# Kernel tuning notes

Hardware: AMD Instinct MI355X
Metric: run time of the kernel (lower is better)

## Reference

```python
import jax, jax.numpy as jnp
import numpy as np

B, S, D, H = 4, 2048, 1024, 16
DH = D // H


def setup_inputs() -> dict:
    key = jax.random.key(0)
    kq, kk, kv, kw, kb = jax.random.split(key, 5)
    queries = jax.random.normal(kq, (B, S, D), dtype=jnp.float32)
    keys = jax.random.normal(kk, (B, S, D), dtype=jnp.float32)
    values = jax.random.normal(kv, (B, S, D), dtype=jnp.float32)
    # True = masked-out padding position; mask the last 64 keys of batch 0
    kpm = np.zeros((B, S), dtype=bool)
    kpm[0, -64:] = True
    key_padding_mask = jnp.asarray(kpm)
    W_O = jax.random.normal(kw, (D, D), dtype=jnp.float32) / np.sqrt(D)
    b_O = jax.random.normal(kb, (D,), dtype=jnp.float32) * 0.01
    return {"queries": queries, "keys": keys, "values": values,
            "key_padding_mask": key_padding_mask, "W_O": W_O, "b_O": b_O}


def reference(queries, keys, values, key_padding_mask, W_O, b_O):
    batch, len_q, d_model = queries.shape
    len_k = keys.shape[1]
    # [B, H, S, DH]
    q = queries.reshape(batch, len_q, H, DH).transpose(0, 2, 1, 3)
    k = keys.reshape(batch, len_k, H, DH).transpose(0, 2, 1, 3)
    v = values.reshape(batch, len_k, H, DH).transpose(0, 2, 1, 3)
    sim = jnp.einsum('bhqd,bhkd->bhqk', q, k) / jnp.sqrt(jnp.float32(DH))
    neg_inf = jnp.finfo(sim.dtype).min
    # padding mask: True means masked
    sim = jnp.where(key_padding_mask[:, None, None, :], neg_inf, sim)
    # causal mask (is_causal=True)
    causal = jnp.tril(jnp.ones((len_q, len_k), dtype=bool))
    sim = jnp.where(causal[None, None], sim, neg_inf)
    attn = jax.nn.softmax(sim, axis=-1)
    out = jnp.einsum('bhqk,bhkd->bhqd', attn, v)  # [B, H, Sq, DH]
    out = out.transpose(0, 2, 1, 3).reshape(batch, len_q, d_model)
    return out @ W_O.T + b_O
```

## Files before the change

kernel.cpp:

```cpp
#include <hip/hip_runtime.h>
#include <hip/hip_bf16.h>

#define B_ 4
#define S_ 2048
#define D_ 1024
#define H_ 16
#define DH_ 64

typedef __attribute__((ext_vector_type(8))) short bf16x8;
typedef __attribute__((ext_vector_type(4))) float f32x4;
typedef __attribute__((ext_vector_type(16))) float f32x16;
typedef __attribute__((ext_vector_type(2))) int v2i;
typedef unsigned int uint32;

__device__ __forceinline__ unsigned short f2bf(float f) {
  unsigned int u = __float_as_uint(f);
  u += 0x7FFFu + ((u >> 16) & 1u);
  return (unsigned short)(u >> 16);
}

__device__ __forceinline__ uint32 pk2(float lo, float hi) {
  return __builtin_amdgcn_perm(__float_as_uint(hi), __float_as_uint(lo), 0x07060302u);
}

__device__ __forceinline__ float half_add(float v) {
  v2i r = __builtin_amdgcn_permlane32_swap(__float_as_int(v), __float_as_int(v), false, false);
  return __int_as_float(r[0]) + __int_as_float(r[1]);
}

__global__ void prep_kernel(const float* __restrict__ k, const float* __restrict__ w,
                            const int* __restrict__ kpm, const float* __restrict__ v,
                            ushort* __restrict__ Kb, ushort* __restrict__ Wb,
                            float* __restrict__ MF, int* __restrict__ anyM,
                            ushort* __restrict__ Vt) {
  __shared__ ushort tile[64][68];
  const int bid = blockIdx.x;
  const int t = threadIdx.x;
  if (bid < 8192) {
    int i = bid * 256 + t;
    float4 a = ((const float4*)k)[i];
    ushort4 r;
    r.x = f2bf(a.x); r.y = f2bf(a.y); r.z = f2bf(a.z); r.w = f2bf(a.w);
    ((ushort4*)Kb)[i] = r;
  } else if (bid < 9216) {
    int i = (bid - 8192) * 256 + t;
    float4 a = ((const float4*)w)[i];
    ushort4 r;
    r.x = f2bf(a.x); r.y = f2bf(a.y); r.z = f2bf(a.z); r.w = f2bf(a.w);
    ((ushort4*)Wb)[i] = r;
  } else if (bid < 9248) {
    int i = (bid - 9216) * 256 + t;
    int m = kpm[i];
    MF[i] = m ? -1e30f : 0.0f;
    unsigned long long bal = __ballot(m != 0);
    if ((i & 63) == 0) anyM[i >> 6] = (bal != 0ull) ? 1 : 0;
  } else {
    int bx = bid - 9248;
    int bh = bx >> 5;
    int s0 = (bx & 31) << 6;
    int b = bh >> 4, h = bh & 15;
#pragma unroll
    for (int it = 0; it < 16; ++it) {
      int r = it * 4 + (t >> 6);
      int c = t & 63;
      float x = v[(size_t)(b * S_ + s0 + r) * D_ + h * DH_ + c];
      tile[r][c] = f2bf(x);
    }
    __syncthreads();
#pragma unroll
    for (int it = 0; it < 16; ++it) {
      int d = it * 4 + (t >> 6);
      int s = t & 63;
      Vt[(size_t)(bh * DH_ + d) * S_ + s0 + s] = tile[s][d];
    }
  }
}

__global__ __launch_bounds__(256, 2) void attn_fwd(
    const float* __restrict__ q, const ushort* __restrict__ Kb,
    const ushort* __restrict__ Vt, const float* __restrict__ MF,
    const int* __restrict__ anyM, ushort* __restrict__ AO) {
  __shared__ ushort Klds[2][2][64 * 64];
  __shared__ ushort Vlds[2][2][64 * 64];

  const int d_ = blockIdx.x;
  const int l_ = (d_ & 7) * 64 + (d_ >> 3);
  const int xx = l_ & 7;
  const int h = (l_ >> 3) & 15;
  const int b = l_ >> 7;

  const int tid = threadIdx.x;
  const int wv = tid >> 6, ln = tid & 63;
  const int q32 = ln & 31;
  const int hi = ln >> 5;
  const int l7 = ln & 7, l3 = ln >> 3;
  const float SC = 0.18033688011112042f;
  const int cr4 = 4 * hi;

  const ushort* Kg = Kb + (size_t)b * S_ * D_ + h * DH_;
  const ushort* Vg = Vt + (size_t)((b * H_ + h) * DH_) * S_;

  bf16x8 kst[4], vst[4];
  const int wrow0 = 16 * wv + l3;
  const int wss = (l7 ^ l3) * 8;

  f32x16 zz;
#pragma unroll
  for (int i = 0; i < 16; ++i) zz[i] = 0.f;

  auto loadTile = [&](int kt) {
#pragma unroll
    for (int hh = 0; hh < 2; ++hh)
#pragma unroll
      for (int p = 0; p < 2; ++p) {
        int row = wrow0 + 8 * p;
        kst[2 * hh + p] = *(const bf16x8*)(Kg + (size_t)(kt * 128 + hh * 64 + row) * D_ + l7 * 8);
        vst[2 * hh + p] = *(const bf16x8*)(Vg + (size_t)row * S_ + kt * 128 + hh * 64 + l7 * 8);
      }
  };
  auto writeTile = [&](int buf) {
#pragma unroll
    for (int hh = 0; hh < 2; ++hh)
#pragma unroll
      for (int p = 0; p < 2; ++p) {
        int row = wrow0 + 8 * p;
        *(bf16x8*)(&Klds[buf][hh][row * 64 + wss]) = kst[2 * hh + p];
        *(bf16x8*)(&Vlds[buf][hh][row * 64 + wss]) = vst[2 * hh + p];
      }
  };
  auto packTile = [&](const f32x16& pv, bf16x8* out) {
#pragma unroll
    for (int kk = 0; kk < 2; ++kk) {
      uint32 a  = pk2(pv[8 * kk + 0], pv[8 * kk + 1]);
      uint32 c  = pk2(pv[8 * kk + 2], pv[8 * kk + 3]);
      uint32 bb = pk2(pv[8 * kk + 4], pv[8 * kk + 5]);
      uint32 dd = pk2(pv[8 * kk + 6], pv[8 * kk + 7]);
      v2i r0 = __builtin_amdgcn_permlane32_swap((int)a, (int)bb, false, false);
      v2i r1 = __builtin_amdgcn_permlane32_swap((int)c, (int)dd, false, false);
      union { uint32 u[4]; bf16x8 v; } w;
      w.u[0] = (uint32)r0[0]; w.u[1] = (uint32)r1[0];
      w.u[2] = (uint32)r0[1]; w.u[3] = (uint32)r1[1];
      out[kk] = w.v;
    }
  };

  for (int half = 0; half < 2; ++half) {
    const int q0 = (half ? (15 - xx) : xx) * 128;
    const int qw0 = q0 + wv * 32;
    const int qb = qw0 >> 5;

    bf16x8 qf[4];
    {
      const float* qp = q + (size_t)(b * S_ + qw0 + q32) * D_ + h * DH_ + hi * 8;
#pragma unroll
      for (int j = 0; j < 4; ++j) {
        float4 x0 = *(const float4*)(qp + 16 * j);
        float4 x1 = *(const float4*)(qp + 16 * j + 4);
        bf16x8 t;
        t[0] = (short)f2bf(x0.x * SC); t[1] = (short)f2bf(x0.y * SC);
        t[2] = (short)f2bf(x0.z * SC); t[3] = (short)f2bf(x0.w * SC);
        t[4] = (short)f2bf(x1.x * SC); t[5] = (short)f2bf(x1.y * SC);
        t[6] = (short)f2bf(x1.z * SC); t[7] = (short)f2bf(x1.w * SC);
        qf[j] = t;
      }
    }

    f32x16 ot0, ot1;
#pragma unroll
    for (int i = 0; i < 16; ++i) { ot0[i] = 0.f; ot1[i] = 0.f; }
    float l_run = 0.f;

    auto full64 = [&](int cur, int hh) {
      const ushort* Kl = &Klds[cur][hh][0];
      const ushort* Vl = &Vlds[cur][hh][0];
      f32x16 s0v, s1v;
      __builtin_amdgcn_s_setprio(1);
#pragma unroll
      for (int j = 0; j < 4; ++j) {
        bf16x8 kf = *(const bf16x8*)(&Kl[q32 * 64 + (((2 * j + hi) ^ l7) * 8)]);
        s0v = __builtin_amdgcn_mfma_f32_32x32x16_bf16(kf, qf[j], j ? s0v : zz, 0, 0, 0);
      }
#pragma unroll
      for (int j = 0; j < 4; ++j) {
        bf16x8 kf = *(const bf16x8*)(&Kl[(32 + q32) * 64 + (((2 * j + hi) ^ l7) * 8)]);
        s1v = __builtin_amdgcn_mfma_f32_32x32x16_bf16(kf, qf[j], j ? s1v : zz, 0, 0, 0);
      }
      __builtin_amdgcn_s_setprio(0);
      float rsa = 0.f, rsb = 0.f;
#pragma unroll
      for (int r = 0; r < 16; ++r) {
        float p0 = __builtin_amdgcn_exp2f(s0v[r]); s0v[r] = p0;
        float p1 = __builtin_amdgcn_exp2f(s1v[r]); s1v[r] = p1;
        if (r & 1) { rsb += p0; rsb += p1; } else { rsa += p0; rsa += p1; }
      }
      l_run += half_add(rsa + rsb);

      bf16x8 pa[4];
      packTile(s0v, &pa[0]);
      packTile(s1v, &pa[2]);
      __builtin_amdgcn_s_setprio(1);
#pragma unroll
      for (int dt = 0; dt < 2; ++dt) {
        f32x16& ot = dt ? ot1 : ot0;
        const int rowb = (dt * 32 + q32) * 64;
        bf16x8 v0 = *(const bf16x8*)(&Vl[rowb + (((0 + hi) ^ l7) * 8)]);
        ot = __builtin_amdgcn_mfma_f32_32x32x16_bf16(v0, pa[0], ot, 0, 0, 0);
        bf16x8 v1 = *(const bf16x8*)(&Vl[rowb + (((2 + hi) ^ l7) * 8)]);
        ot = __builtin_amdgcn_mfma_f32_32x32x16_bf16(v1, pa[1], ot, 0, 0, 0);
        bf16x8 v2 = *(const bf16x8*)(&Vl[rowb + (((4 + hi) ^ l7) * 8)]);
        ot = __builtin_amdgcn_mfma_f32_32x32x16_bf16(v2, pa[2], ot, 0, 0, 0);
        bf16x8 v3 = *(const bf16x8*)(&Vl[rowb + (((6 + hi) ^ l7) * 8)]);
        ot = __builtin_amdgcn_mfma_f32_32x32x16_bf16(v3, pa[3], ot, 0, 0, 0);
      }
      __builtin_amdgcn_s_setprio(0);
    };

    auto generic64 = [&](int t64, int cur, int hh) {
      const int k0 = t64 * 64;
      const ushort* Kl = &Klds[cur][hh][0];
      const ushort* Vl = &Vlds[cur][hh][0];
      const bool a0 = (2 * t64) <= qb, a1 = (2 * t64 + 1) <= qb;
      if (!(a0 || a1)) return;
      const bool dg0 = (2 * t64) == qb, dg1 = (2 * t64 + 1) == qb;
      const int flag = anyM[b * 32 + t64];

      f32x16 s0v, s1v;
      __builtin_amdgcn_s_setprio(1);
      if (a0) {
#pragma unroll
        for (int j = 0; j < 4; ++j) {
          bf16x8 kf = *(const bf16x8*)(&Kl[q32 * 64 + (((2 * j + hi) ^ l7) * 8)]);
          s0v = __builtin_amdgcn_mfma_f32_32x32x16_bf16(kf, qf[j], j ? s0v : zz, 0, 0, 0);
        }
      }
      if (a1) {
#pragma unroll
        for (int j = 0; j < 4; ++j) {
          bf16x8 kf = *(const bf16x8*)(&Kl[(32 + q32) * 64 + (((2 * j + hi) ^ l7) * 8)]);
          s1v = __builtin_amdgcn_mfma_f32_32x32x16_bf16(kf, qf[j], j ? s1v : zz, 0, 0, 0);
        }
      }
      __builtin_amdgcn_s_setprio(0);

      float rsa = 0.f, rsb = 0.f;
      if (a0) {
#pragma unroll
        for (int r = 0; r < 16; ++r) {
          int cr = (r & 3) + 8 * (r >> 2) + cr4;
          float s = s0v[r];
          if (flag) s += MF[b * S_ + k0 + cr];
          if (dg0 && cr > q32) s = -3.0e38f;
          float p = __builtin_amdgcn_exp2f(s);
          s0v[r] = p;
          if (r & 1) rsb += p; else rsa += p;
        }
      }
      if (a1) {
#pragma unroll
        for (int r = 0; r < 16; ++r) {
          int cr = (r & 3) + 8 * (r >> 2) + cr4;
          float s = s1v[r];
          if (flag) s += MF[b * S_ + k0 + 32 + cr];
          if (dg1 && cr > q32) s = -3.0e38f;
          float p = __builtin_amdgcn_exp2f(s);
          s1v[r] = p;
          if (r & 1) rsb += p; else rsa += p;
        }
      }
      l_run += half_add(rsa + rsb);

      bf16x8 pa[4];
      if (a0) packTile(s0v, &pa[0]);
      if (a1) packTile(s1v, &pa[2]);

      __builtin_amdgcn_s_setprio(1);
#pragma unroll
      for (int dt = 0; dt < 2; ++dt) {
        f32x16& ot = dt ? ot1 : ot0;
        const int rowb = (dt * 32 + q32) * 64;
        if (a0) {
          bf16x8 v0 = *(const bf16x8*)(&Vl[rowb + (((0 + hi) ^ l7) * 8)]);
          ot = __builtin_amdgcn_mfma_f32_32x32x16_bf16(v0, pa[0], ot, 0, 0, 0);
          bf16x8 v1 = *(const bf16x8*)(&Vl[rowb + (((2 + hi) ^ l7) * 8)]);
          ot = __builtin_amdgcn_mfma_f32_32x32x16_bf16(v1, pa[1], ot, 0, 0, 0);
        }
        if (a1) {
          bf16x8 v2 = *(const bf16x8*)(&Vl[rowb + (((4 + hi) ^ l7) * 8)]);
          ot = __builtin_amdgcn_mfma_f32_32x32x16_bf16(v2, pa[2], ot, 0, 0, 0);
          bf16x8 v3 = *(const bf16x8*)(&Vl[rowb + (((6 + hi) ^ l7) * 8)]);
          ot = __builtin_amdgcn_mfma_f32_32x32x16_bf16(v3, pa[3], ot, 0, 0, 0);
        }
      }
      __builtin_amdgcn_s_setprio(0);
    };

    const int M = (q0 >> 7) + 1;
    loadTile(0);
    writeTile(0);
    if (M > 1) loadTile(1);
    __syncthreads();

    for (int tt = 0; tt < M; ++tt) {
      const int cur = tt & 1;
      if (tt + 1 < M) writeTile(cur ^ 1);
      if (tt + 2 < M) loadTile(tt + 2);
      if (tt < M - 1) {
        const int f0 = anyM[b * 32 + 2 * tt] | anyM[b * 32 + 2 * tt + 1];
        if (f0) { generic64(2 * tt, cur, 0); generic64(2 * tt + 1, cur, 1); }
        else { full64(cur, 0); full64(cur, 1); }
      } else {
        generic64(2 * tt, cur, 0);
        generic64(2 * tt + 1, cur, 1);
      }
      __syncthreads();
    }

    const float inv = __builtin_amdgcn_rcpf(l_run);
    ushort* tb = ((ushort*)Klds) + wv * 2048;
#pragma unroll
    for (int dt = 0; dt < 2; ++dt) {
      const f32x16& ot = dt ? ot1 : ot0;
#pragma unroll
      for (int rp = 0; rp < 8; ++rp) {
        int r0 = rp * 2;
        int d0 = dt * 32 + (r0 & 3) + 8 * (r0 >> 2) + cr4;
        uint32 w = pk2(ot[r0] * inv, ot[r0 + 1] * inv);
        int e = q32 * 64 + (((d0 >> 3) ^ (q32 & 7)) * 8) + (d0 & 7);
        *(uint32*)(&tb[e]) = w;
      }
    }
    __syncthreads();
#pragma unroll
    for (int it = 0; it < 4; ++it) {
      int qq = it * 8 + l3;
      bf16x8 val = *(const bf16x8*)(&tb[qq * 64 + ((l7 ^ (qq & 7)) * 8)]);
      *(bf16x8*)(AO + (size_t)(b * S_ + qw0 + qq) * D_ + h * DH_ + l7 * 8) = val;
    }
    __syncthreads();
  }
}

__global__ __launch_bounds__(256, 2) void gemm_out(
    const ushort* __restrict__ A, const ushort* __restrict__ Wb,
    const float* __restrict__ bO, float* __restrict__ out) {
  __shared__ ushort Al[2][128 * 64];
  __shared__ ushort Wl[2][128 * 64];
  const int dd = blockIdx.x;
  const int m0 = (dd & 63) * 128;
  const int n0 = (dd >> 6) * 128;
  const int tid = threadIdx.x;
  const int wv = tid >> 6, ln = tid & 63;
  const int r16 = ln & 15, g = ln >> 4;
  const int wm = wv >> 1, wn = wv & 1;
  const int trow = tid >> 3, tslot = tid & 7;
  f32x4 acc[4][4] = {};
  bf16x8 ast[4], wst[4];

  auto stageReg = [&](int kc) {
    const int kk = kc * 64;
#pragma unroll
    for (int p = 0; p < 4; ++p) {
      int row = trow + 32 * p;
      ast[p] = *(const bf16x8*)(A + (size_t)(m0 + row) * D_ + kk + tslot * 8);
      wst[p] = *(const bf16x8*)(Wb + (size_t)(n0 + row) * D_ + kk + tslot * 8);
    }
  };
  auto writeL = [&](int buf) {
#pragma unroll
    for (int p = 0; p < 4; ++p) {
      int row = trow + 32 * p;
      int soff = (tslot ^ (row & 7)) * 8;
      *(bf16x8*)(&Al[buf][row * 64 + soff]) = ast[p];
      *(bf16x8*)(&Wl[buf][row * 64 + soff]) = wst[p];
    }
  };

  stageReg(0);
  writeL(0);
  stageReg(1);
  __syncthreads();

  for (int kc = 0; kc < 16; ++kc) {
    const int cur = kc & 1;
    if (kc + 1 < 16) writeL(cur ^ 1);
    if (kc + 2 < 16) stageReg(kc + 2);
#pragma unroll
    for (int hh = 0; hh < 2; ++hh) {
      bf16x8 af[4], wf[4];
#pragma unroll
      for (int m = 0; m < 4; ++m) {
        int row = 64 * wm + 16 * m + r16;
        af[m] = *(const bf16x8*)(&Al[cur][row * 64 + (((4 * hh + g) ^ (row & 7)) * 8)]);
      }
#pragma unroll
      for (int n = 0; n < 4; ++n) {
        int row = 64 * wn + 16 * n + r16;
        wf[n] = *(const bf16x8*)(&Wl[cur][row * 64 + (((4 * hh + g) ^ (row & 7)) * 8)]);
      }
#pragma unroll
      for (int m = 0; m < 4; ++m)
#pragma unroll
        for (int n = 0; n < 4; ++n)
          acc[m][n] = __builtin_amdgcn_mfma_f32_16x16x32_bf16(af[m], wf[n], acc[m][n], 0, 0, 0);
    }
    __syncthreads();
  }

#pragma unroll
  for (int n = 0; n < 4; ++n) {
    float bb = bO[n0 + 32 * wn * 2 + 16 * n + r16];
#pragma unroll
    for (int m = 0; m < 4; ++m) {
#pragma unroll
      for (int j = 0; j < 4; ++j) {
        out[(size_t)(m0 + 64 * wm + 16 * m + 4 * g + j) * D_ + n0 + 64 * wn + 16 * n + r16] =
            acc[m][n][j] + bb;
      }
    }
  }
}

extern "C" void kernel_launch(void* const* d_in, const int* in_sizes, int n_in,
                              void* d_out, int out_size, void* d_ws, size_t ws_size,
                              hipStream_t stream) {
  const float* q = (const float*)d_in[0];
  const float* k = (const float*)d_in[1];
  const float* v = (const float*)d_in[2];
  const int* kpm = (const int*)d_in[3];
  const float* W = (const float*)d_in[4];
  const float* bO = (const float*)d_in[5];

  char* ws = (char*)d_ws;
  const size_t SZ = (size_t)B_ * S_ * D_ * 2;
  ushort* Kb = (ushort*)ws;
  ushort* Vt = (ushort*)(ws + SZ);
  ushort* AO = (ushort*)(ws + 2 * SZ);
  ushort* Wb = (ushort*)(ws + 3 * SZ);
  float* MF = (float*)(ws + 3 * SZ + (size_t)D_ * D_ * 2);
  int* anyM = (int*)(ws + 3 * SZ + (size_t)D_ * D_ * 2 + (size_t)B_ * S_ * 4);

  prep_kernel<<<11296, 256, 0, stream>>>(k, W, kpm, v, Kb, Wb, MF, anyM, Vt);
  attn_fwd<<<512, 256, 0, stream>>>(q, Kb, Vt, MF, anyM, AO);
  gemm_out<<<512, 256, 0, stream>>>(AO, Wb, bO, (float*)d_out);
}
```

Baseline: 96.17 us.

## Split paired causal query tiles into separate blocks with 64-key tiles

Each attention block previously handled two query tiles, an early one paired with a late one for causal load balance, and streamed 128-key tiles. Now each of 1024 blocks handles one query tile, ordered from longest to shortest, and streams 64-key double-buffered tiles, which halves shared memory per block. This is meant to raise occupancy and parallelism and to let the scheduler balance the uneven causal work, at the cost of more blocks and more barriers per key step. The gemm bias index expression is also rewritten to an equivalent form.

```diff
diff --git a/kernel.cpp b/kernel.cpp
--- a/kernel.cpp
+++ b/kernel.cpp
@@ -80,14 +80,15 @@
     const float* __restrict__ q, const ushort* __restrict__ Kb,
     const ushort* __restrict__ Vt, const float* __restrict__ MF,
     const int* __restrict__ anyM, ushort* __restrict__ AO) {
-  __shared__ ushort Klds[2][2][64 * 64];
-  __shared__ ushort Vlds[2][2][64 * 64];
+  __shared__ ushort Klds[2][64 * 64];
+  __shared__ ushort Vlds[2][64 * 64];
 
   const int d_ = blockIdx.x;
-  const int l_ = (d_ & 7) * 64 + (d_ >> 3);
-  const int xx = l_ & 7;
-  const int h = (l_ >> 3) & 15;
-  const int b = l_ >> 7;
+  const int l_ = (d_ & 7) * 128 + (d_ >> 3);
+  const int xx = l_ & 15;
+  const int h = (l_ >> 4) & 15;
+  const int b = l_ >> 8;
+  const int q0 = (15 - xx) * 128;
 
   const int tid = threadIdx.x;
   const int wv = tid >> 6, ln = tid & 63;
@@ -100,7 +101,7 @@
   const ushort* Kg = Kb + (size_t)b * S_ * D_ + h * DH_;
   const ushort* Vg = Vt + (size_t)((b * H_ + h) * DH_) * S_;
 
-  bf16x8 kst[4], vst[4];
+  bf16x8 kst[2], vst[2];
   const int wrow0 = 16 * wv + l3;
   const int wss = (l7 ^ l3) * 8;
 
@@ -110,23 +111,19 @@
 
   auto loadTile = [&](int kt) {
 #pragma unroll
-    for (int hh = 0; hh < 2; ++hh)
-#pragma unroll
-      for (int p = 0; p < 2; ++p) {
-        int row = wrow0 + 8 * p;
-        kst[2 * hh + p] = *(const bf16x8*)(Kg + (size_t)(kt * 128 + hh * 64 + row) * D_ + l7 * 8);
-        vst[2 * hh + p] = *(const bf16x8*)(Vg + (size_t)row * S_ + kt * 128 + hh * 64 + l7 * 8);
-      }
+    for (int p = 0; p < 2; ++p) {
+      int row = wrow0 + 8 * p;
+      kst[p] = *(const bf16x8*)(Kg + (size_t)(kt * 64 + row) * D_ + l7 * 8);
+      vst[p] = *(const bf16x8*)(Vg + (size_t)row * S_ + kt * 64 + l7 * 8);
+    }
   };
   auto writeTile = [&](int buf) {
 #pragma unroll
-    for (int hh = 0; hh < 2; ++hh)
-#pragma unroll
-      for (int p = 0; p < 2; ++p) {
-        int row = wrow0 + 8 * p;
-        *(bf16x8*)(&Klds[buf][hh][row * 64 + wss]) = kst[2 * hh + p];
-        *(bf16x8*)(&Vlds[buf][hh][row * 64 + wss]) = vst[2 * hh + p];
-      }
+    for (int p = 0; p < 2; ++p) {
+      int row = wrow0 + 8 * p;
+      *(bf16x8*)(&Klds[buf][row * 64 + wss]) = kst[p];
+      *(bf16x8*)(&Vlds[buf][row * 64 + wss]) = vst[p];
+    }
   };
   auto packTile = [&](const f32x16& pv, bf16x8* out) {
 #pragma unroll
@@ -144,199 +141,193 @@
     }
   };
 
-  for (int half = 0; half < 2; ++half) {
-    const int q0 = (half ? (15 - xx) : xx) * 128;
-    const int qw0 = q0 + wv * 32;
-    const int qb = qw0 >> 5;
-
-    bf16x8 qf[4];
-    {
-      const float* qp = q + (size_t)(b * S_ + qw0 + q32) * D_ + h * DH_ + hi * 8;
-#pragma unroll
-      for (int j = 0; j < 4; ++j) {
-        float4 x0 = *(const float4*)(qp + 16 * j);
-        float4 x1 = *(const float4*)(qp + 16 * j + 4);
-        bf16x8 t;
-        t[0] = (short)f2bf(x0.x * SC); t[1] = (short)f2bf(x0.y * SC);
-        t[2] = (short)f2bf(x0.z * SC); t[3] = (short)f2bf(x0.w * SC);
-        t[4] = (short)f2bf(x1.x * SC); t[5] = (short)f2bf(x1.y * SC);
-        t[6] = (short)f2bf(x1.z * SC); t[7] = (short)f2bf(x1.w * SC);
-        qf[j] = t;
-      }
-    }
-
-    f32x16 ot0, ot1;
-#pragma unroll
-    for (int i = 0; i < 16; ++i) { ot0[i] = 0.f; ot1[i] = 0.f; }
-    float l_run = 0.f;
-
-    auto full64 = [&](int cur, int hh) {
-      const ushort* Kl = &Klds[cur][hh][0];
-      const ushort* Vl = &Vlds[cur][hh][0];
-      f32x16 s0v, s1v;
-      __builtin_amdgcn_s_setprio(1);
+  const int qw0 = q0 + wv * 32;
+  const int qb = qw0 >> 5;
+
+  bf16x8 qf[4];
+  {
+    const float* qp = q + (size_t)(b * S_ + qw0 + q32) * D_ + h * DH_ + hi * 8;
+#pragma unroll
+    for (int j = 0; j < 4; ++j) {
+      float4 x0 = *(const float4*)(qp + 16 * j);
+      float4 x1 = *(const float4*)(qp + 16 * j + 4);
+      bf16x8 t;
+      t[0] = (short)f2bf(x0.x * SC); t[1] = (short)f2bf(x0.y * SC);
+      t[2] = (short)f2bf(x0.z * SC); t[3] = (short)f2bf(x0.w * SC);
+      t[4] = (short)f2bf(x1.x * SC); t[5] = (short)f2bf(x1.y * SC);
+      t[6] = (short)f2bf(x1.z * SC); t[7] = (short)f2bf(x1.w * SC);
+      qf[j] = t;
+    }
+  }
+
+  f32x16 ot0, ot1;
+#pragma unroll
+  for (int i = 0; i < 16; ++i) { ot0[i] = 0.f; ot1[i] = 0.f; }
+  float l_run = 0.f;
+
+  auto full64 = [&](int cur) {
+    const ushort* Kl = &Klds[cur][0];
+    const ushort* Vl = &Vlds[cur][0];
+    f32x16 s0v, s1v;
+    __builtin_amdgcn_s_setprio(1);
+#pragma unroll
+    for (int j = 0; j < 4; ++j) {
+      bf16x8 kf = *(const bf16x8*)(&Kl[q32 * 64 + (((2 * j + hi) ^ l7) * 8)]);
+      s0v = __builtin_amdgcn_mfma_f32_32x32x16_bf16(kf, qf[j], j ? s0v : zz, 0, 0, 0);
+    }
+#pragma unroll
+    for (int j = 0; j < 4; ++j) {
+      bf16x8 kf = *(const bf16x8*)(&Kl[(32 + q32) * 64 + (((2 * j + hi) ^ l7) * 8)]);
+      s1v = __builtin_amdgcn_mfma_f32_32x32x16_bf16(kf, qf[j], j ? s1v : zz, 0, 0, 0);
+    }
+    __builtin_amdgcn_s_setprio(0);
+    float rsa = 0.f, rsb = 0.f;
+#pragma unroll
+    for (int r = 0; r < 16; ++r) {
+      float p0 = __builtin_amdgcn_exp2f(s0v[r]); s0v[r] = p0;
+      float p1 = __builtin_amdgcn_exp2f(s1v[r]); s1v[r] = p1;
+      if (r & 1) { rsb += p0; rsb += p1; } else { rsa += p0; rsa += p1; }
+    }
+    l_run += half_add(rsa + rsb);
+
+    bf16x8 pa[4];
+    packTile(s0v, &pa[0]);
+    packTile(s1v, &pa[2]);
+    __builtin_amdgcn_s_setprio(1);
+#pragma unroll
+    for (int dt = 0; dt < 2; ++dt) {
+      f32x16& ot = dt ? ot1 : ot0;
+      const int rowb = (dt * 32 + q32) * 64;
+      bf16x8 v0 = *(const bf16x8*)(&Vl[rowb + (((0 + hi) ^ l7) * 8)]);
+      ot = __builtin_amdgcn_mfma_f32_32x32x16_bf16(v0, pa[0], ot, 0, 0, 0);
+      bf16x8 v1 = *(const bf16x8*)(&Vl[rowb + (((2 + hi) ^ l7) * 8)]);
+      ot = __builtin_amdgcn_mfma_f32_32x32x16_bf16(v1, pa[1], ot, 0, 0, 0);
+      bf16x8 v2 = *(const bf16x8*)(&Vl[rowb + (((4 + hi) ^ l7) * 8)]);
+      ot = __builtin_amdgcn_mfma_f32_32x32x16_bf16(v2, pa[2], ot, 0, 0, 0);
+      bf16x8 v3 = *(const bf16x8*)(&Vl[rowb + (((6 + hi) ^ l7) * 8)]);
+      ot = __builtin_amdgcn_mfma_f32_32x32x16_bf16(v3, pa[3], ot, 0, 0, 0);
+    }
+    __builtin_amdgcn_s_setprio(0);
+  };
+
+  auto generic64 = [&](int t64, int cur) {
+    const int k0 = t64 * 64;
+    const ushort* Kl = &Klds[cur][0];
+    const ushort* Vl = &Vlds[cur][0];
+    const bool a0 = (2 * t64) <= qb, a1 = (2 * t64 + 1) <= qb;
+    if (!(a0 || a1)) return;
+    const bool dg0 = (2 * t64) == qb, dg1 = (2 * t64 + 1) == qb;
+    const int flag = anyM[b * 32 + t64];
+
+    f32x16 s0v, s1v;
+    __builtin_amdgcn_s_setprio(1);
+    if (a0) {
 #pragma unroll
       for (int j = 0; j < 4; ++j) {
         bf16x8 kf = *(const bf16x8*)(&Kl[q32 * 64 + (((2 * j + hi) ^ l7) * 8)]);
         s0v = __builtin_amdgcn_mfma_f32_32x32x16_bf16(kf, qf[j], j ? s0v : zz, 0, 0, 0);
       }
+    }
+    if (a1) {
 #pragma unroll
       for (int j = 0; j < 4; ++j) {
         bf16x8 kf = *(const bf16x8*)(&Kl[(32 + q32) * 64 + (((2 * j + hi) ^ l7) * 8)]);
         s1v = __builtin_amdgcn_mfma_f32_32x32x16_bf16(kf, qf[j], j ? s1v : zz, 0, 0, 0);
       }
-      __builtin_amdgcn_s_setprio(0);
-      float rsa = 0.f, rsb = 0.f;
+    }
+    __builtin_amdgcn_s_setprio(0);
+
+    float rsa = 0.f, rsb = 0.f;
+    if (a0) {
 #pragma unroll
       for (int r = 0; r < 16; ++r) {
-        float p0 = __builtin_amdgcn_exp2f(s0v[r]); s0v[r] = p0;
-        float p1 = __builtin_amdgcn_exp2f(s1v[r]); s1v[r] = p1;
-        if (r & 1) { rsb += p0; rsb += p1; } else { rsa += p0; rsa += p1; }
-      }
-      l_run += half_add(rsa + rsb);
-
-      bf16x8 pa[4];
-      packTile(s0v, &pa[0]);
-      packTile(s1v, &pa[2]);
-      __builtin_amdgcn_s_setprio(1);
-#pragma unroll
-      for (int dt = 0; dt < 2; ++dt) {
-        f32x16& ot = dt ? ot1 : ot0;
-        const int rowb = (dt * 32 + q32) * 64;
+        int cr = (r & 3) + 8 * (r >> 2) + cr4;
+        float s = s0v[r];
+        if (flag) s += MF[b * S_ + k0 + cr];
+        if (dg0 && cr > q32) s = -3.0e38f;
+        float p = __builtin_amdgcn_exp2f(s);
+        s0v[r] = p;
+        if (r & 1) rsb += p; else rsa += p;
+      }
+    }
+    if (a1) {
+#pragma unroll
+      for (int r = 0; r < 16; ++r) {
+        int cr = (r & 3) + 8 * (r >> 2) + cr4;
+        float s = s1v[r];
+        if (flag) s += MF[b * S_ + k0 + 32 + cr];
+        if (dg1 && cr > q32) s = -3.0e38f;
+        float p = __builtin_amdgcn_exp2f(s);
+        s1v[r] = p;
+        if (r & 1) rsb += p; else rsa += p;
+      }
+    }
+    l_run += half_add(rsa + rsb);
+
+    bf16x8 pa[4];
+    if (a0) packTile(s0v, &pa[0]);
+    if (a1) packTile(s1v, &pa[2]);
+
+    __builtin_amdgcn_s_setprio(1);
+#pragma unroll
+    for (int dt = 0; dt < 2; ++dt) {
+      f32x16& ot = dt ? ot1 : ot0;
+      const int rowb = (dt * 32 + q32) * 64;
+      if (a0) {
         bf16x8 v0 = *(const bf16x8*)(&Vl[rowb + (((0 + hi) ^ l7) * 8)]);
         ot = __builtin_amdgcn_mfma_f32_32x32x16_bf16(v0, pa[0], ot, 0, 0, 0);
         bf16x8 v1 = *(const bf16x8*)(&Vl[rowb + (((2 + hi) ^ l7) * 8)]);
         ot = __builtin_amdgcn_mfma_f32_32x32x16_bf16(v1, pa[1], ot, 0, 0, 0);
+      }
+      if (a1) {
         bf16x8 v2 = *(const bf16x8*)(&Vl[rowb + (((4 + hi) ^ l7) * 8)]);
         ot = __builtin_amdgcn_mfma_f32_32x32x16_bf16(v2, pa[2], ot, 0, 0, 0);
         bf16x8 v3 = *(const bf16x8*)(&Vl[rowb + (((6 + hi) ^ l7) * 8)]);
         ot = __builtin_amdgcn_mfma_f32_32x32x16_bf16(v3, pa[3], ot, 0, 0, 0);
       }
-      __builtin_amdgcn_s_setprio(0);
-    };
-
-    auto generic64 = [&](int t64, int cur, int hh) {
-      const int k0 = t64 * 64;
-      const ushort* Kl = &Klds[cur][hh][0];
-      const ushort* Vl = &Vlds[cur][hh][0];
-      const bool a0 = (2 * t64) <= qb, a1 = (2 * t64 + 1) <= qb;
-      if (!(a0 || a1)) return;
-      const bool dg0 = (2 * t64) == qb, dg1 = (2 * t64 + 1) == qb;
-      const int flag = anyM[b * 32 + t64];
-
-      f32x16 s0v, s1v;
-      __builtin_amdgcn_s_setprio(1);
-      if (a0) {
-#pragma unroll
-        for (int j = 0; j < 4; ++j) {
-          bf16x8 kf = *(const bf16x8*)(&Kl[q32 * 64 + (((2 * j + hi) ^ l7) * 8)]);
-          s0v = __builtin_amdgcn_mfma_f32_32x32x16_bf16(kf, qf[j], j ? s0v : zz, 0, 0, 0);
-        }
-      }
-      if (a1) {
-#pragma unroll
-        for (int j = 0; j < 4; ++j) {
-          bf16x8 kf = *(const bf16x8*)(&Kl[(32 + q32) * 64 + (((2 * j + hi) ^ l7) * 8)]);
-          s1v = __builtin_amdgcn_mfma_f32_32x32x16_bf16(kf, qf[j], j ? s1v : zz, 0, 0, 0);
-        }
-      }
-      __builtin_amdgcn_s_setprio(0);
-
-      float rsa = 0.f, rsb = 0.f;
-      if (a0) {
-#pragma unroll
-        for (int r = 0; r < 16; ++r) {
-          int cr = (r & 3) + 8 * (r >> 2) + cr4;
-          float s = s0v[r];
-          if (flag) s += MF[b * S_ + k0 + cr];
-          if (dg0 && cr > q32) s = -3.0e38f;
-          float p = __builtin_amdgcn_exp2f(s);
-          s0v[r] = p;
-          if (r & 1) rsb += p; else rsa += p;
-        }
-      }
-      if (a1) {
-#pragma unroll
-        for (int r = 0; r < 16; ++r) {
-          int cr = (r & 3) + 8 * (r >> 2) + cr4;
-          float s = s1v[r];
-          if (flag) s += MF[b * S_ + k0 + 32 + cr];
-          if (dg1 && cr > q32) s = -3.0e38f;
-          float p = __builtin_amdgcn_exp2f(s);
-          s1v[r] = p;
-          if (r & 1) rsb += p; else rsa += p;
-        }
-      }
-      l_run += half_add(rsa + rsb);
-
-      bf16x8 pa[4];
-      if (a0) packTile(s0v, &pa[0]);
-      if (a1) packTile(s1v, &pa[2]);
-
-      __builtin_amdgcn_s_setprio(1);
-#pragma unroll
-      for (int dt = 0; dt < 2; ++dt) {
-        f32x16& ot = dt ? ot1 : ot0;
-        const int rowb = (dt * 32 + q32) * 64;
-        if (a0) {
-          bf16x8 v0 = *(const bf16x8*)(&Vl[rowb + (((0 + hi) ^ l7) * 8)]);
-          ot = __builtin_amdgcn_mfma_f32_32x32x16_bf16(v0, pa[0], ot, 0, 0, 0);
-          bf16x8 v1 = *(const bf16x8*)(&Vl[rowb + (((2 + hi) ^ l7) * 8)]);
-          ot = __builtin_amdgcn_mfma_f32_32x32x16_bf16(v1, pa[1], ot, 0, 0, 0);
-        }
-        if (a1) {
-          bf16x8 v2 = *(const bf16x8*)(&Vl[rowb + (((4 + hi) ^ l7) * 8)]);
-          ot = __builtin_amdgcn_mfma_f32_32x32x16_bf16(v2, pa[2], ot, 0, 0, 0);
-          bf16x8 v3 = *(const bf16x8*)(&Vl[rowb + (((6 + hi) ^ l7) * 8)]);
-          ot = __builtin_amdgcn_mfma_f32_32x32x16_bf16(v3, pa[3], ot, 0, 0, 0);
-        }
-      }
-      __builtin_amdgcn_s_setprio(0);
-    };
-
-    const int M = (q0 >> 7) + 1;
-    loadTile(0);
-    writeTile(0);
-    if (M > 1) loadTile(1);
+    }
+    __builtin_amdgcn_s_setprio(0);
+  };
+
+  const int nkb = (q0 >> 6) + 2;
+  loadTile(0);
+  writeTile(0);
+  loadTile(1);
+  __syncthreads();
+
+  for (int t = 0; t < nkb; ++t) {
+    const int cur = t & 1;
+    if (t + 1 < nkb) writeTile(cur ^ 1);
+    if (t + 2 < nkb) loadTile(t + 2);
+    if (t < nkb - 2) {
+      if (anyM[b * 32 + t]) generic64(t, cur);
+      else full64(cur);
+    } else {
+      generic64(t, cur);
+    }
     __syncthreads();
-
-    for (int tt = 0; tt < M; ++tt) {
-      const int cur = tt & 1;
-      if (tt + 1 < M) writeTile(cur ^ 1);
-      if (tt + 2 < M) loadTile(tt + 2);
-      if (tt < M - 1) {
-        const int f0 = anyM[b * 32 + 2 * tt] | anyM[b * 32 + 2 * tt + 1];
-        if (f0) { generic64(2 * tt, cur, 0); generic64(2 * tt + 1, cur, 1); }
-        else { full64(cur, 0); full64(cur, 1); }
-      } else {
-        generic64(2 * tt, cur, 0);
-        generic64(2 * tt + 1, cur, 1);
-      }
-      __syncthreads();
-    }
-
-    const float inv = __builtin_amdgcn_rcpf(l_run);
-    ushort* tb = ((ushort*)Klds) + wv * 2048;
-#pragma unroll
-    for (int dt = 0; dt < 2; ++dt) {
-      const f32x16& ot = dt ? ot1 : ot0;
-#pragma unroll
-      for (int rp = 0; rp < 8; ++rp) {
-        int r0 = rp * 2;
-        int d0 = dt * 32 + (r0 & 3) + 8 * (r0 >> 2) + cr4;
-        uint32 w = pk2(ot[r0] * inv, ot[r0 + 1] * inv);
-        int e = q32 * 64 + (((d0 >> 3) ^ (q32 & 7)) * 8) + (d0 & 7);
-        *(uint32*)(&tb[e]) = w;
-      }
-    }
-    __syncthreads();
-#pragma unroll
-    for (int it = 0; it < 4; ++it) {
-      int qq = it * 8 + l3;
-      bf16x8 val = *(const bf16x8*)(&tb[qq * 64 + ((l7 ^ (qq & 7)) * 8)]);
-      *(bf16x8*)(AO + (size_t)(b * S_ + qw0 + qq) * D_ + h * DH_ + l7 * 8) = val;
-    }
-    __syncthreads();
+  }
+
+  const float inv = __builtin_amdgcn_rcpf(l_run);
+  ushort* tb = ((ushort*)Klds) + wv * 2048;
+#pragma unroll
+  for (int dt = 0; dt < 2; ++dt) {
+    const f32x16& ot = dt ? ot1 : ot0;
+#pragma unroll
+    for (int rp = 0; rp < 8; ++rp) {
+      int r0 = rp * 2;
+      int d0 = dt * 32 + (r0 & 3) + 8 * (r0 >> 2) + cr4;
+      uint32 w = pk2(ot[r0] * inv, ot[r0 + 1] * inv);
+      int e = q32 * 64 + (((d0 >> 3) ^ (q32 & 7)) * 8) + (d0 & 7);
+      *(uint32*)(&tb[e]) = w;
+    }
+  }
+  __syncthreads();
+#pragma unroll
+  for (int it = 0; it < 4; ++it) {
+    int qq = it * 8 + l3;
+    bf16x8 val = *(const bf16x8*)(&tb[qq * 64 + ((l7 ^ (qq & 7)) * 8)]);
+    *(bf16x8*)(AO + (size_t)(b * S_ + qw0 + qq) * D_ + h * DH_ + l7 * 8) = val;
   }
 }
 
@@ -408,7 +399,7 @@
 
 #pragma unroll
   for (int n = 0; n < 4; ++n) {
-    float bb = bO[n0 + 32 * wn * 2 + 16 * n + r16];
+    float bb = bO[n0 + 64 * wn + 16 * n + r16];
 #pragma unroll
     for (int m = 0; m < 4; ++m) {
 #pragma unroll
@@ -440,6 +431,6 @@
   int* anyM = (int*)(ws + 3 * SZ + (size_t)D_ * D_ * 2 + (size_t)B_ * S_ * 4);
 
   prep_kernel<<<11296, 256, 0, stream>>>(k, W, kpm, v, Kb, Wb, MF, anyM, Vt);
-  attn_fwd<<<512, 256, 0, stream>>>(q, Kb, Vt, MF, anyM, AO);
+  attn_fwd<<<1024, 256, 0, stream>>>(q, Kb, Vt, MF, anyM, AO);
   gemm_out<<<512, 256, 0, stream>>>(AO, Wb, bO, (float*)d_out);
 }
```

After: 116.3 us. 21.0% more time.

## Process both paired causal query tiles in one K/V sweep

Applied to the files above, without the earlier changes.

The attention block previously handled its two query tiles (a short and a long causal row pair) in two sequential passes, loading K/V tiles twice. Now both Q tiles are kept in registers and a single pass over the longer tile's K/V range serves both, sharing each LDS tile load. This roughly halves K/V global loads and the barrier count per block, at the cost of doubling the output accumulator registers, which may reduce occupancy or cause spills. The bias index expression in the output GEMM is rewritten into an equivalent form.

```diff
diff --git a/kernel.cpp b/kernel.cpp
--- a/kernel.cpp
+++ b/kernel.cpp
@@ -144,182 +144,196 @@
     }
   };
 
-  for (int half = 0; half < 2; ++half) {
-    const int q0 = (half ? (15 - xx) : xx) * 128;
-    const int qw0 = q0 + wv * 32;
-    const int qb = qw0 >> 5;
-
-    bf16x8 qf[4];
-    {
-      const float* qp = q + (size_t)(b * S_ + qw0 + q32) * D_ + h * DH_ + hi * 8;
-#pragma unroll
-      for (int j = 0; j < 4; ++j) {
-        float4 x0 = *(const float4*)(qp + 16 * j);
-        float4 x1 = *(const float4*)(qp + 16 * j + 4);
-        bf16x8 t;
-        t[0] = (short)f2bf(x0.x * SC); t[1] = (short)f2bf(x0.y * SC);
-        t[2] = (short)f2bf(x0.z * SC); t[3] = (short)f2bf(x0.w * SC);
-        t[4] = (short)f2bf(x1.x * SC); t[5] = (short)f2bf(x1.y * SC);
-        t[6] = (short)f2bf(x1.z * SC); t[7] = (short)f2bf(x1.w * SC);
-        qf[j] = t;
-      }
-    }
-
-    f32x16 ot0, ot1;
-#pragma unroll
-    for (int i = 0; i < 16; ++i) { ot0[i] = 0.f; ot1[i] = 0.f; }
-    float l_run = 0.f;
-
-    auto full64 = [&](int cur, int hh) {
-      const ushort* Kl = &Klds[cur][hh][0];
-      const ushort* Vl = &Vlds[cur][hh][0];
-      f32x16 s0v, s1v;
-      __builtin_amdgcn_s_setprio(1);
+  const int q0A = xx * 128, q0B = (15 - xx) * 128;
+  const int qw0A = q0A + wv * 32, qw0B = q0B + wv * 32;
+  const int qbA = qw0A >> 5, qbB = qw0B >> 5;
+
+  bf16x8 qfA[4], qfB[4];
+  auto loadQ = [&](int qw0, bf16x8* qf) {
+    const float* qp = q + (size_t)(b * S_ + qw0 + q32) * D_ + h * DH_ + hi * 8;
+#pragma unroll
+    for (int j = 0; j < 4; ++j) {
+      float4 x0 = *(const float4*)(qp + 16 * j);
+      float4 x1 = *(const float4*)(qp + 16 * j + 4);
+      bf16x8 t;
+      t[0] = (short)f2bf(x0.x * SC); t[1] = (short)f2bf(x0.y * SC);
+      t[2] = (short)f2bf(x0.z * SC); t[3] = (short)f2bf(x0.w * SC);
+      t[4] = (short)f2bf(x1.x * SC); t[5] = (short)f2bf(x1.y * SC);
+      t[6] = (short)f2bf(x1.z * SC); t[7] = (short)f2bf(x1.w * SC);
+      qf[j] = t;
+    }
+  };
+  loadQ(qw0A, qfA);
+  loadQ(qw0B, qfB);
+
+  f32x16 oA0, oA1, oB0, oB1;
+#pragma unroll
+  for (int i = 0; i < 16; ++i) { oA0[i] = 0.f; oA1[i] = 0.f; oB0[i] = 0.f; oB1[i] = 0.f; }
+  float lA = 0.f, lB = 0.f;
+
+  auto fullG = [&](int cur, int hh, const bf16x8* qf, f32x16& o0, f32x16& o1, float& lr) {
+    const ushort* Kl = &Klds[cur][hh][0];
+    const ushort* Vl = &Vlds[cur][hh][0];
+    f32x16 s0v, s1v;
+    __builtin_amdgcn_s_setprio(1);
+#pragma unroll
+    for (int j = 0; j < 4; ++j) {
+      bf16x8 kf = *(const bf16x8*)(&Kl[q32 * 64 + (((2 * j + hi) ^ l7) * 8)]);
+      s0v = __builtin_amdgcn_mfma_f32_32x32x16_bf16(kf, qf[j], j ? s0v : zz, 0, 0, 0);
+    }
+#pragma unroll
+    for (int j = 0; j < 4; ++j) {
+      bf16x8 kf = *(const bf16x8*)(&Kl[(32 + q32) * 64 + (((2 * j + hi) ^ l7) * 8)]);
+      s1v = __builtin_amdgcn_mfma_f32_32x32x16_bf16(kf, qf[j], j ? s1v : zz, 0, 0, 0);
+    }
+    __builtin_amdgcn_s_setprio(0);
+    float rsa = 0.f, rsb = 0.f;
+#pragma unroll
+    for (int r = 0; r < 16; ++r) {
+      float p0 = __builtin_amdgcn_exp2f(s0v[r]); s0v[r] = p0;
+      float p1 = __builtin_amdgcn_exp2f(s1v[r]); s1v[r] = p1;
+      if (r & 1) { rsb += p0; rsb += p1; } else { rsa += p0; rsa += p1; }
+    }
+    lr += half_add(rsa + rsb);
+
+    bf16x8 pa[4];
+    packTile(s0v, &pa[0]);
+    packTile(s1v, &pa[2]);
+    __builtin_amdgcn_s_setprio(1);
+#pragma unroll
+    for (int dt = 0; dt < 2; ++dt) {
+      f32x16& ot = dt ? o1 : o0;
+      const int rowb = (dt * 32 + q32) * 64;
+      bf16x8 v0 = *(const bf16x8*)(&Vl[rowb + (((0 + hi) ^ l7) * 8)]);
+      ot = __builtin_amdgcn_mfma_f32_32x32x16_bf16(v0, pa[0], ot, 0, 0, 0);
+      bf16x8 v1 = *(const bf16x8*)(&Vl[rowb + (((2 + hi) ^ l7) * 8)]);
+      ot = __builtin_amdgcn_mfma_f32_32x32x16_bf16(v1, pa[1], ot, 0, 0, 0);
+      bf16x8 v2 = *(const bf16x8*)(&Vl[rowb + (((4 + hi) ^ l7) * 8)]);
+      ot = __builtin_amdgcn_mfma_f32_32x32x16_bf16(v2, pa[2], ot, 0, 0, 0);
+      bf16x8 v3 = *(const bf16x8*)(&Vl[rowb + (((6 + hi) ^ l7) * 8)]);
+      ot = __builtin_amdgcn_mfma_f32_32x32x16_bf16(v3, pa[3], ot, 0, 0, 0);
+    }
+    __builtin_amdgcn_s_setprio(0);
+  };
+
+  auto genericG = [&](int t64, int cur, int hh, const bf16x8* qf,
+                      f32x16& o0, f32x16& o1, float& lr, int qb) {
+    const int k0 = t64 * 64;
+    const ushort* Kl = &Klds[cur][hh][0];
+    const ushort* Vl = &Vlds[cur][hh][0];
+    const bool a0 = (2 * t64) <= qb, a1 = (2 * t64 + 1) <= qb;
+    if (!(a0 || a1)) return;
+    const bool dg0 = (2 * t64) == qb, dg1 = (2 * t64 + 1) == qb;
+    const int flag = anyM[b * 32 + t64];
+
+    f32x16 s0v, s1v;
+    __builtin_amdgcn_s_setprio(1);
+    if (a0) {
 #pragma unroll
       for (int j = 0; j < 4; ++j) {
         bf16x8 kf = *(const bf16x8*)(&Kl[q32 * 64 + (((2 * j + hi) ^ l7) * 8)]);
         s0v = __builtin_amdgcn_mfma_f32_32x32x16_bf16(kf, qf[j], j ? s0v : zz, 0, 0, 0);
       }
+    }
+    if (a1) {
 #pragma unroll
       for (int j = 0; j < 4; ++j) {
         bf16x8 kf = *(const bf16x8*)(&Kl[(32 + q32) * 64 + (((2 * j + hi) ^ l7) * 8)]);
         s1v = __builtin_amdgcn_mfma_f32_32x32x16_bf16(kf, qf[j], j ? s1v : zz, 0, 0, 0);
       }
-      __builtin_amdgcn_s_setprio(0);
-      float rsa = 0.f, rsb = 0.f;
+    }
+    __builtin_amdgcn_s_setprio(0);
+
+    float rsa = 0.f, rsb = 0.f;
+    if (a0) {
 #pragma unroll
       for (int r = 0; r < 16; ++r) {
-        float p0 = __builtin_amdgcn_exp2f(s0v[r]); s0v[r] = p0;
-        float p1 = __builtin_amdgcn_exp2f(s1v[r]); s1v[r] = p1;
-        if (r & 1) { rsb += p0; rsb += p1; } else { rsa += p0; rsa += p1; }
-      }
-      l_run += half_add(rsa + rsb);
-
-      bf16x8 pa[4];
-      packTile(s0v, &pa[0]);
-      packTile(s1v, &pa[2]);
-      __builtin_amdgcn_s_setprio(1);
-#pragma unroll
-      for (int dt = 0; dt < 2; ++dt) {
-        f32x16& ot = dt ? ot1 : ot0;
-        const int rowb = (dt * 32 + q32) * 64;
+        int cr = (r & 3) + 8 * (r >> 2) + cr4;
+        float s = s0v[r];
+        if (flag) s += MF[b * S_ + k0 + cr];
+        if (dg0 && cr > q32) s = -3.0e38f;
+        float p = __builtin_amdgcn_exp2f(s);
+        s0v[r] = p;
+        if (r & 1) rsb += p; else rsa += p;
+      }
+    }
+    if (a1) {
+#pragma unroll
+      for (int r = 0; r < 16; ++r) {
+        int cr = (r & 3) + 8 * (r >> 2) + cr4;
+        float s = s1v[r];
+        if (flag) s += MF[b * S_ + k0 + 32 + cr];
+        if (dg1 && cr > q32) s = -3.0e38f;
+        float p = __builtin_amdgcn_exp2f(s);
+        s1v[r] = p;
+        if (r & 1) rsb += p; else rsa += p;
+      }
+    }
+    lr += half_add(rsa + rsb);
+
+    bf16x8 pa[4];
+    if (a0) packTile(s0v, &pa[0]);
+    if (a1) packTile(s1v, &pa[2]);
+
+    __builtin_amdgcn_s_setprio(1);
+#pragma unroll
+    for (int dt = 0; dt < 2; ++dt) {
+      f32x16& ot = dt ? o1 : o0;
+      const int rowb = (dt * 32 + q32) * 64;
+      if (a0) {
         bf16x8 v0 = *(const bf16x8*)(&Vl[rowb + (((0 + hi) ^ l7) * 8)]);
         ot = __builtin_amdgcn_mfma_f32_32x32x16_bf16(v0, pa[0], ot, 0, 0, 0);
         bf16x8 v1 = *(const bf16x8*)(&Vl[rowb + (((2 + hi) ^ l7) * 8)]);
         ot = __builtin_amdgcn_mfma_f32_32x32x16_bf16(v1, pa[1], ot, 0, 0, 0);
+      }
+      if (a1) {
         bf16x8 v2 = *(const bf16x8*)(&Vl[rowb + (((4 + hi) ^ l7) * 8)]);
         ot = __builtin_amdgcn_mfma_f32_32x32x16_bf16(v2, pa[2], ot, 0, 0, 0);
         bf16x8 v3 = *(const bf16x8*)(&Vl[rowb + (((6 + hi) ^ l7) * 8)]);
         ot = __builtin_amdgcn_mfma_f32_32x32x16_bf16(v3, pa[3], ot, 0, 0, 0);
       }
-      __builtin_amdgcn_s_setprio(0);
-    };
-
-    auto generic64 = [&](int t64, int cur, int hh) {
-      const int k0 = t64 * 64;
-      const ushort* Kl = &Klds[cur][hh][0];
-      const ushort* Vl = &Vlds[cur][hh][0];
-      const bool a0 = (2 * t64) <= qb, a1 = (2 * t64 + 1) <= qb;
-      if (!(a0 || a1)) return;
-      const bool dg0 = (2 * t64) == qb, dg1 = (2 * t64 + 1) == qb;
-      const int flag = anyM[b * 32 + t64];
-
-      f32x16 s0v, s1v;
-      __builtin_amdgcn_s_setprio(1);
-      if (a0) {
-#pragma unroll
-        for (int j = 0; j < 4; ++j) {
-          bf16x8 kf = *(const bf16x8*)(&Kl[q32 * 64 + (((2 * j + hi) ^ l7) * 8)]);
-          s0v = __builtin_amdgcn_mfma_f32_32x32x16_bf16(kf, qf[j], j ? s0v : zz, 0, 0, 0);
-        }
-      }
-      if (a1) {
-#pragma unroll
-        for (int j = 0; j < 4; ++j) {
-          bf16x8 kf = *(const bf16x8*)(&Kl[(32 + q32) * 64 + (((2 * j + hi) ^ l7) * 8)]);
-          s1v = __builtin_amdgcn_mfma_f32_32x32x16_bf16(kf, qf[j], j ? s1v : zz, 0, 0, 0);
-        }
-      }
-      __builtin_amdgcn_s_setprio(0);
-
-      float rsa = 0.f, rsb = 0.f;
-      if (a0) {
-#pragma unroll
-        for (int r = 0; r < 16; ++r) {
-          int cr = (r & 3) + 8 * (r >> 2) + cr4;
-          float s = s0v[r];
-          if (flag) s += MF[b * S_ + k0 + cr];
-          if (dg0 && cr > q32) s = -3.0e38f;
-          float p = __builtin_amdgcn_exp2f(s);
-          s0v[r] = p;
-          if (r & 1) rsb += p; else rsa += p;
-        }
-      }
-      if (a1) {
-#pragma unroll
-        for (int r = 0; r < 16; ++r) {
-          int cr = (r & 3) + 8 * (r >> 2) + cr4;
-          float s = s1v[r];
-          if (flag) s += MF[b * S_ + k0 + 32 + cr];
-          if (dg1 && cr > q32) s = -3.0e38f;
-          float p = __builtin_amdgcn_exp2f(s);
-          s1v[r] = p;
-          if (r & 1) rsb += p; else rsa += p;
-        }
-      }
-      l_run += half_add(rsa + rsb);
-
-      bf16x8 pa[4];
-      if (a0) packTile(s0v, &pa[0]);
-      if (a1) packTile(s1v, &pa[2]);
-
-      __builtin_amdgcn_s_setprio(1);
-#pragma unroll
-      for (int dt = 0; dt < 2; ++dt) {
-        f32x16& ot = dt ? ot1 : ot0;
-        const int rowb = (dt * 32 + q32) * 64;
-        if (a0) {
-          bf16x8 v0 = *(const bf16x8*)(&Vl[rowb + (((0 + hi) ^ l7) * 8)]);
-          ot = __builtin_amdgcn_mfma_f32_32x32x16_bf16(v0, pa[0], ot, 0, 0, 0);
-          bf16x8 v1 = *(const bf16x8*)(&Vl[rowb + (((2 + hi) ^ l7) * 8)]);
-          ot = __builtin_amdgcn_mfma_f32_32x32x16_bf16(v1, pa[1], ot, 0, 0, 0);
-        }
-        if (a1) {
-          bf16x8 v2 = *(const bf16x8*)(&Vl[rowb + (((4 + hi) ^ l7) * 8)]);
-          ot = __builtin_amdgcn_mfma_f32_32x32x16_bf16(v2, pa[2], ot, 0, 0, 0);
-          bf16x8 v3 = *(const bf16x8*)(&Vl[rowb + (((6 + hi) ^ l7) * 8)]);
-          ot = __builtin_amdgcn_mfma_f32_32x32x16_bf16(v3, pa[3], ot, 0, 0, 0);
-        }
-      }
-      __builtin_amdgcn_s_setprio(0);
-    };
-
-    const int M = (q0 >> 7) + 1;
-    loadTile(0);
-    writeTile(0);
-    if (M > 1) loadTile(1);
+    }
+    __builtin_amdgcn_s_setprio(0);
+  };
+
+  const int MB = 16 - xx;
+  const int nkbA = 2 * xx + 2;
+  const int nkbB = 2 * MB;
+
+  loadTile(0);
+  writeTile(0);
+  if (MB > 1) loadTile(1);
+  __syncthreads();
+
+  for (int tt = 0; tt < MB; ++tt) {
+    const int cur = tt & 1;
+    if (tt + 1 < MB) writeTile(cur ^ 1);
+    if (tt + 2 < MB) loadTile(tt + 2);
+#pragma unroll
+    for (int hh = 0; hh < 2; ++hh) {
+      const int t64 = 2 * tt + hh;
+      if (t64 < nkbA - 2) {
+        if (anyM[b * 32 + t64]) genericG(t64, cur, hh, qfA, oA0, oA1, lA, qbA);
+        else fullG(cur, hh, qfA, oA0, oA1, lA);
+      } else if (t64 < nkbA) {
+        genericG(t64, cur, hh, qfA, oA0, oA1, lA, qbA);
+      }
+      if (t64 < nkbB - 2) {
+        if (anyM[b * 32 + t64]) genericG(t64, cur, hh, qfB, oB0, oB1, lB, qbB);
+        else fullG(cur, hh, qfB, oB0, oB1, lB);
+      } else {
+        genericG(t64, cur, hh, qfB, oB0, oB1, lB, qbB);
+      }
+    }
     __syncthreads();
-
-    for (int tt = 0; tt < M; ++tt) {
-      const int cur = tt & 1;
-      if (tt + 1 < M) writeTile(cur ^ 1);
-      if (tt + 2 < M) loadTile(tt + 2);
-      if (tt < M - 1) {
-        const int f0 = anyM[b * 32 + 2 * tt] | anyM[b * 32 + 2 * tt + 1];
-        if (f0) { generic64(2 * tt, cur, 0); generic64(2 * tt + 1, cur, 1); }
-        else { full64(cur, 0); full64(cur, 1); }
-      } else {
-        generic64(2 * tt, cur, 0);
-        generic64(2 * tt + 1, cur, 1);
-      }
-      __syncthreads();
-    }
-
-    const float inv = __builtin_amdgcn_rcpf(l_run);
-    ushort* tb = ((ushort*)Klds) + wv * 2048;
+  }
+
+  ushort* tb = ((ushort*)Klds) + wv * 2048;
+  auto epi = [&](const f32x16& o0, const f32x16& o1, float lr, int qw0) {
+    const float inv = __builtin_amdgcn_rcpf(lr);
 #pragma unroll
     for (int dt = 0; dt < 2; ++dt) {
-      const f32x16& ot = dt ? ot1 : ot0;
+      const f32x16& ot = dt ? o1 : o0;
 #pragma unroll
       for (int rp = 0; rp < 8; ++rp) {
         int r0 = rp * 2;
@@ -336,8 +350,10 @@
       bf16x8 val = *(const bf16x8*)(&tb[qq * 64 + ((l7 ^ (qq & 7)) * 8)]);
       *(bf16x8*)(AO + (size_t)(b * S_ + qw0 + qq) * D_ + h * DH_ + l7 * 8) = val;
     }
-    __syncthreads();
-  }
+  };
+  epi(oA0, oA1, lA, qw0A);
+  __syncthreads();
+  epi(oB0, oB1, lB, qw0B);
 }
 
 __global__ __launch_bounds__(256, 2) void gemm_out(
@@ -408,7 +424,7 @@
 
 #pragma unroll
   for (int n = 0; n < 4; ++n) {
-    float bb = bO[n0 + 32 * wn * 2 + 16 * n + r16];
+    float bb = bO[n0 + 64 * wn + 16 * n + r16];
 #pragma unroll
     for (int m = 0; m < 4; ++m) {
 #pragma unroll
```

Result: slower. 98.21 us (+2.1%).
